# Kernel tuning notes

Measured on AMD Instinct MI355X. Metric: run time of the kernel, lower is better.

The kernel has to match this reference:

```python
import jax, jax.numpy as jnp
import numpy as np

B, S, D = 1, 2048, 1024
NH, NKV, WS = 8, 2, 64
HD = D // NH  # 128
E, HDIM, TOPK = 16, 512, 2
FP16_MIN = -65504.0
EPS = 1e-6
AUX_COEFF = 1e-5


def rmsnorm(x, w):
    return x * jax.lax.rsqrt(jnp.mean(x * x, axis=-1, keepdims=True) + EPS) * w


def setup_inputs() -> dict:
    key = jax.random.key(0)
    ks = jax.random.split(key, 24)
    r = lambda k, shape, fan: jax.random.normal(k, shape, dtype=jnp.float32) * (1.0 / np.sqrt(fan))
    return {
        "x": jax.random.normal(ks[0], (B, S, D), dtype=jnp.float32),
        "norm1_w": jnp.ones((D,), jnp.float32),
        "wq": r(ks[1], (D, NH * HD), D), "bq": jnp.zeros((NH * HD,), jnp.float32),
        "wk": r(ks[2], (D, NKV * HD), D), "bk": jnp.zeros((NKV * HD,), jnp.float32),
        "wv": r(ks[3], (D, NKV * HD), D), "bv": jnp.zeros((NKV * HD,), jnp.float32),
        "wo": r(ks[4], (NH * HD, D), NH * HD), "bo": jnp.zeros((D,), jnp.float32),
        "sink_bias": jnp.zeros((), jnp.float32),
        "norm2_w": jnp.ones((D,), jnp.float32),
        "router_w": r(ks[5], (D, E), D), "router_b": jnp.zeros((E,), jnp.float32),
        "w1": r(ks[6], (E, D, HDIM), D), "b1": jnp.zeros((E, HDIM), jnp.float32),
        "w2": r(ks[7], (E, HDIM, D), HDIM), "b2": jnp.zeros((E, D), jnp.float32),
    }


def reference(x, norm1_w, wq, bq, wk, bk, wv, bv, wo, bo, sink_bias,
              norm2_w, router_w, router_b, w1, b1, w2, b2):
    # ---- sliding-window attention with sink softmax ----
    h = rmsnorm(x, norm1_w)
    q = (h @ wq + bq).reshape(B, S, NH, HD).transpose(0, 2, 1, 3)    # [B,NH,S,HD]
    k = (h @ wk + bk).reshape(B, S, NKV, HD).transpose(0, 2, 1, 3)   # [B,NKV,S,HD]
    v = (h @ wv + bv).reshape(B, S, NKV, HD).transpose(0, 2, 1, 3)
    k = jnp.repeat(k, NH // NKV, axis=1)  # GQA expand -> [B,NH,S,HD]
    v = jnp.repeat(v, NH // NKV, axis=1)
    scores = jnp.einsum('bhqd,bhkd->bhqk', q, k) / np.sqrt(HD)
    i = jnp.arange(S)[:, None]
    j = jnp.arange(S)[None, :]
    band = (i - j >= 0) & (i - j <= WS - 1)  # causal sliding window
    scores = jnp.where(band, scores, FP16_MIN)
    m = jnp.maximum(jnp.max(scores, axis=-1, keepdims=True), sink_bias)
    ew = jnp.exp(scores - m)
    denom = jnp.sum(ew, axis=-1, keepdims=True) + jnp.exp(sink_bias - m)
    attn = ew / denom
    out = jnp.einsum('bhqk,bhkd->bhqd', attn, v).transpose(0, 2, 1, 3).reshape(B, S, D)
    x = x + (out @ wo + bo)

    # ---- MoE FFN ----
    h2 = rmsnorm(x, norm2_w)
    xf = h2.reshape(-1, D)                                  # [N,D]
    logits = (xf @ router_w + router_b) / 0.1               # [N,E]
    top_v, top_i = jax.lax.top_k(logits, TOPK)              # [N,k]
    top_w = jax.nn.softmax(top_v, axis=-1)
    probs = jax.nn.softmax(logits, axis=-1)
    aux_loss = jnp.sum(jnp.sum(probs, axis=0) ** 2) / E * AUX_COEFF
    # combine weights per (token, expert)
    gate = jnp.sum(jax.nn.one_hot(top_i, E, dtype=xf.dtype) * top_w[..., None], axis=1)  # [N,E]
    hmid = jax.nn.silu(jnp.einsum('nd,edh->neh', xf, w1) + b1)   # [N,E,H]
    y = jnp.einsum('neh,ehd->ned', hmid, w2) + b2                # [N,E,D]
    ffn = jnp.einsum('ne,ned->nd', gate, y)
    x = x + ffn.reshape(B, S, D)
    return x, aux_loss
```

## Files before the change

kernel.cpp:

```cpp
#include <hip/hip_runtime.h>
#include <hip/hip_bf16.h>

#define S     2048
#define D     1024
#define NH    8
#define NKV   2
#define HD    128
#define WS_   64
#define E_    16
#define HDIM  512
#define TOPK  2
#define NTOK  S
#define NSLOT (S*TOPK)
#define QKV_M (D + 2*NKV*HD)
#define KOFF  D
#define VOFF  (D + NKV*HD)
#define QB    8
#define WROWS (QB + WS_ - 1)
#define KPITCH 73
#define VPADF  132

typedef __attribute__((ext_vector_type(8))) short bf16x8;
typedef __attribute__((ext_vector_type(4))) float floatx4;

__device__ inline short f2bf(float f) {
    __hip_bfloat16 b = __float2bfloat16(f);
    return *reinterpret_cast<short*>(&b);
}

__global__ __launch_bounds__(256) void tconv_all(
    const float* __restrict__ wq, const float* __restrict__ wk,
    const float* __restrict__ wv, const float* __restrict__ wo,
    const float* __restrict__ w1, const float* __restrict__ w2,
    const float* __restrict__ bq, const float* __restrict__ bk,
    const float* __restrict__ bv, const float* __restrict__ router_w,
    short* __restrict__ wqkvT, short* __restrict__ woT,
    short* __restrict__ w1T, short* __restrict__ w2T,
    float* __restrict__ bqkv, float* __restrict__ rwT,
    const float* __restrict__ x, const float* __restrict__ norm1_w,
    short* __restrict__ h_bf)
{
    int id = blockIdx.x;
    if (id >= 18982) {
        int row = id - 18982, t = threadIdx.x;
        float4 v = ((const float4*)(x + (size_t)row * D))[t];
        float ss = v.x*v.x + v.y*v.y + v.z*v.z + v.w*v.w;
        #pragma unroll
        for (int off = 32; off; off >>= 1) ss += __shfl_xor(ss, off, 64);
        __shared__ float red[4];
        if ((t & 63) == 0) red[t >> 6] = ss;
        __syncthreads();
        float total = red[0] + red[1] + red[2] + red[3];
        float scale = rsqrtf(total * (1.0f / (float)D) + 1e-6f);
        float4 wv4 = ((const float4*)norm1_w)[t];
        short4 ob;
        ob.x = f2bf(v.x * scale * wv4.x); ob.y = f2bf(v.y * scale * wv4.y);
        ob.z = f2bf(v.z * scale * wv4.z); ob.w = f2bf(v.w * scale * wv4.w);
        ((short4*)(h_bf + (size_t)row * D))[t] = ob;
        return;
    }
    if (id >= 18950) {
        int ky = id - 18950;
        int t = threadIdx.x;
        int r = t >> 4, c = t & 15;
        int k0 = ky * 32;
        rwT[c * D + k0 + r]      = router_w[(k0 + r) * E_ + c];
        rwT[c * D + k0 + r + 16] = router_w[(k0 + r + 16) * E_ + c];
        return;
    }
    if (id >= 18944) {
        int t = (id - 18944) * 256 + threadIdx.x;
        if (t < D) bqkv[t] = bq[t];
        else if (t < VOFF) bqkv[t] = bk[t - D];
        else bqkv[t] = bv[t - VOFF];
        return;
    }
    const float* in; short* outp; int K, M, mx, ky;
    if (id < 1024)      { in = wq; outp = wqkvT;                  K = D; M = D;   int l = id;        mx = l & 31; ky = l >> 5; }
    else if (id < 1280) { in = wk; outp = wqkvT + (size_t)KOFF*D; K = D; M = 256; int l = id - 1024; mx = l & 7;  ky = l >> 3; }
    else if (id < 1536) { in = wv; outp = wqkvT + (size_t)VOFF*D; K = D; M = 256; int l = id - 1280; mx = l & 7;  ky = l >> 3; }
    else if (id < 2560) { in = wo; outp = woT;                    K = D; M = D;   int l = id - 1536; mx = l & 31; ky = l >> 5; }
    else if (id < 10752){ int l = id - 2560;  int e = l >> 9; int r = l & 511;
                          in = w1 + (size_t)e * D * HDIM; outp = w1T + (size_t)e * D * HDIM;
                          K = D; M = HDIM; mx = r & 15; ky = r >> 4; }
    else                { int l = id - 10752; int e = l >> 9; int r = l & 511;
                          in = w2 + (size_t)e * D * HDIM; outp = w2T + (size_t)e * D * HDIM;
                          K = HDIM; M = D; mx = r & 31; ky = r >> 5; }
    __shared__ float tile[32][33];
    int t = threadIdx.x, r = t >> 3, c4 = (t & 7) * 4;
    int k0 = ky * 32, m0 = mx * 32;
    float4 v = *(const float4*)&in[(size_t)(k0 + r) * M + m0 + c4];
    tile[r][c4 + 0] = v.x; tile[r][c4 + 1] = v.y;
    tile[r][c4 + 2] = v.z; tile[r][c4 + 3] = v.w;
    __syncthreads();
    short4 o;
    o.x = f2bf(tile[c4 + 0][r]);
    o.y = f2bf(tile[c4 + 1][r]);
    o.z = f2bf(tile[c4 + 2][r]);
    o.w = f2bf(tile[c4 + 3][r]);
    *(short4*)&outp[(size_t)(m0 + r) * K + k0 + c4] = o;
}

#define BT   64
#define BKS  64
#define BUFS (BT * BKS)

__device__ inline void gld16(const short* g, short* l) {
    __builtin_amdgcn_global_load_lds(
        (const __attribute__((address_space(1))) unsigned int*)g,
        (__attribute__((address_space(3))) unsigned int*)l, 16, 0, 0);
}

template <int V>
__global__ __launch_bounds__(256) void mgemm(
    const short* __restrict__ A, const short* __restrict__ Bt,
    const float* __restrict__ bias, float* __restrict__ C,
    short* __restrict__ Cb, const float* __restrict__ res, int K, int M,
    const int* __restrict__ offs, const float* __restrict__ tok_gate,
    const int* __restrict__ tok_map)
{
    int e = (V >= 2) ? blockIdx.z : 0;
    const short* Bte = (V >= 2) ? Bt + (size_t)e * M * K : Bt;
    const float* be  = (V >= 2) ? bias + (size_t)e * M : bias;

    int row_lo, row_hi;
    if (V >= 2) {
        row_lo = offs[e] + blockIdx.y * BT;
        row_hi = offs[e + 1];
        if (row_lo >= row_hi) return;
    } else {
        row_lo = blockIdx.y * BT;
        row_hi = 1 << 30;
    }
    int col0 = blockIdx.x * BT;

    __shared__ __align__(16) short As[2 * BUFS];
    __shared__ __align__(16) short Bs[2 * BUFS];

    int t = threadIdx.x;
    int wave = t >> 6, lane = t & 63;
    int lrow   = lane >> 3;
    int schunk = (lane & 7) ^ lrow;

    const short* aQ[2];
    const short* bQ[2];
    #pragma unroll
    for (int q = 0; q < 2; ++q) {
        int row = q * 32 + wave * 8 + lrow;
        int gr = row_lo + row;
        if (V >= 2 && gr >= row_hi) gr = row_lo;
        const short* arow;
        if (V == 2) arow = A + (size_t)(tok_map[gr] & (NTOK - 1)) * K;
        else        arow = A + (size_t)gr * K;
        aQ[q] = arow + (schunk << 3);
        bQ[q] = Bte + (size_t)(col0 + row) * K + (schunk << 3);
    }

    int rin = lane & 15, quad = lane >> 4;
    int wm = (wave & 1) * 32, wn = (wave >> 1) * 32;

    floatx4 acc[2][2];
    #pragma unroll
    for (int i = 0; i < 2; ++i)
        #pragma unroll
        for (int j = 0; j < 2; ++j)
            acc[i][j] = (floatx4){0.f, 0.f, 0.f, 0.f};

    const int NIT = K >> 6;

    #pragma unroll
    for (int q = 0; q < 2; ++q) {
        gld16(aQ[q], &As[(q * 32 + wave * 8) * BKS]);
        gld16(bQ[q], &Bs[(q * 32 + wave * 8) * BKS]);
    }
    __syncthreads();

    for (int it = 0; it < NIT; ++it) {
        int cur = it & 1, nxt = cur ^ 1;
        if (it + 1 < NIT) {
            int kk = (it + 1) << 6;
            #pragma unroll
            for (int q = 0; q < 2; ++q) {
                gld16(aQ[q] + kk, &As[nxt * BUFS + (q * 32 + wave * 8) * BKS]);
                gld16(bQ[q] + kk, &Bs[nxt * BUFS + (q * 32 + wave * 8) * BKS]);
            }
        }
        const short* Ab = &As[cur * BUFS];
        const short* Bb = &Bs[cur * BUFS];
        #pragma unroll
        for (int s = 0; s < 2; ++s) {
            bf16x8 af[2], bfr[2];
            #pragma unroll
            for (int i = 0; i < 2; ++i) {
                int row = wm + i * 16 + rin;
                af[i] = *(const bf16x8*)&Ab[row * BKS
                        + ((((s << 2) | quad) ^ (rin & 7)) << 3)];
            }
            #pragma unroll
            for (int j = 0; j < 2; ++j) {
                int row = wn + j * 16 + rin;
                bfr[j] = *(const bf16x8*)&Bb[row * BKS
                        + ((((s << 2) | quad) ^ (rin & 7)) << 3)];
            }
            #pragma unroll
            for (int i = 0; i < 2; ++i)
                #pragma unroll
                for (int j = 0; j < 2; ++j)
                    acc[i][j] = __builtin_amdgcn_mfma_f32_16x16x32_bf16(
                        af[i], bfr[j], acc[i][j], 0, 0, 0);
        }
        __syncthreads();
    }

    #pragma unroll
    for (int i = 0; i < 2; ++i) {
        #pragma unroll
        for (int j = 0; j < 2; ++j) {
            int cg = col0 + wn + j * 16 + rin;
            #pragma unroll
            for (int rr = 0; rr < 4; ++rr) {
                int rg = row_lo + wm + i * 16 + quad * 4 + rr;
                float val = acc[i][j][rr];
                if (V == 0) {
                    C[(size_t)rg * M + cg] = val + be[cg];
                } else if (V == 1) {
                    C[(size_t)rg * M + cg] = val + be[cg] + res[(size_t)rg * M + cg];
                } else if (V == 2) {
                    if (rg < row_hi) {
                        float vb_ = val + be[cg];
                        Cb[(size_t)rg * M + cg] = f2bf(vb_ / (1.f + __expf(-vb_)));
                    }
                } else {
                    if (rg < row_hi) {
                        int tok = tok_map[rg] & (NTOK - 1);
                        unsafeAtomicAdd(&C[(size_t)tok * M + cg],
                                        tok_gate[rg] * (val + be[cg]));
                    }
                }
            }
        }
    }
}

__global__ __launch_bounds__(256) void attn_kernel(
    const float* __restrict__ qkv, const float* __restrict__ sink_ptr,
    short* __restrict__ ao)
{
    __shared__ __align__(16) float KT[32 * KPITCH * 4];
    __shared__ __align__(16) float Vs[WROWS * VPADF];
    __shared__ __align__(16) float Ps4[4][64][4];

    int qblk = blockIdx.x;
    int kvh  = blockIdx.y;
    int q0   = qblk * QB;
    int jbase = q0 - (WS_ - 1);

    int t = threadIdx.x;
    int c4 = (t & 31) * 4, c4g = t & 31;
    for (int r = t >> 5; r < WROWS; r += 8) {
        int j = jbase + r;
        float4 kv4 = make_float4(0.f, 0.f, 0.f, 0.f);
        float4 vv4 = make_float4(0.f, 0.f, 0.f, 0.f);
        if (j >= 0) {
            kv4 = *(const float4*)(qkv + (size_t)j * QKV_M + KOFF + kvh * HD + c4);
            vv4 = *(const float4*)(qkv + (size_t)j * QKV_M + VOFF + kvh * HD + c4);
        }
        *(float4*)&KT[(c4g * KPITCH + r) * 4] = kv4;
        *(float4*)&Vs[r * VPADF + c4] = vv4;
    }
    __syncthreads();

    int lane = t & 63, wv = t >> 6;
    float sink = sink_ptr[0];
    const float rscale = 0.08838834764831845f;

    #pragma unroll
    for (int g = 0; g < 2; ++g) {
        int qi = wv * 2 + g;
        int i  = q0 + qi;
        bool valid = (jbase + qi + lane) >= 0;

        float sc[4] = {0.f, 0.f, 0.f, 0.f};
        const float* qbase = qkv + (size_t)i * QKV_M + (kvh * 4) * HD;
        #pragma unroll
        for (int c = 0; c < 32; ++c) {
            float4 kx = *(const float4*)&KT[(c * KPITCH + qi + lane) * 4];
            #pragma unroll
            for (int hh = 0; hh < 4; ++hh) {
                float4 q4 = *(const float4*)(qbase + hh * HD + c * 4);
                sc[hh] += q4.x*kx.x + q4.y*kx.y + q4.z*kx.z + q4.w*kx.w;
            }
        }

        float pn[4];
        #pragma unroll
        for (int hh = 0; hh < 4; ++hh) {
            float s = valid ? sc[hh] * rscale : -1e30f;
            float m = s;
            #pragma unroll
            for (int off = 32; off; off >>= 1) m = fmaxf(m, __shfl_xor(m, off, 64));
            float mf = fmaxf(m, sink);
            float p  = __expf(s - mf);
            float ds = p;
            #pragma unroll
            for (int off = 32; off; off >>= 1) ds += __shfl_xor(ds, off, 64);
            pn[hh] = p / (ds + __expf(sink - mf));
        }
        *(float4*)&Ps4[wv][lane][0] = make_float4(pn[0], pn[1], pn[2], pn[3]);

        float o0=0,o1=0,o2=0,o3=0,o4=0,o5=0,o6=0,o7=0;
        const float* vp = &Vs[qi * VPADF + 2 * lane];
        #pragma unroll
        for (int jj = 0; jj < 64; ++jj) {
            float4 p4 = *(const float4*)&Ps4[wv][jj][0];
            float2 vv = *(const float2*)(vp + jj * VPADF);
            o0 += p4.x * vv.x; o1 += p4.x * vv.y;
            o2 += p4.y * vv.x; o3 += p4.y * vv.y;
            o4 += p4.z * vv.x; o5 += p4.z * vv.y;
            o6 += p4.w * vv.x; o7 += p4.w * vv.y;
        }
        short2 r0; r0.x = f2bf(o0); r0.y = f2bf(o1);
        short2 r1; r1.x = f2bf(o2); r1.y = f2bf(o3);
        short2 r2; r2.x = f2bf(o4); r2.y = f2bf(o5);
        short2 r3; r3.x = f2bf(o6); r3.y = f2bf(o7);
        ((short2*)(ao + (size_t)i * D + (kvh * 4 + 0) * HD))[lane] = r0;
        ((short2*)(ao + (size_t)i * D + (kvh * 4 + 1) * HD))[lane] = r1;
        ((short2*)(ao + (size_t)i * D + (kvh * 4 + 2) * HD))[lane] = r2;
        ((short2*)(ao + (size_t)i * D + (kvh * 4 + 3) * HD))[lane] = r3;
    }
}

__global__ __launch_bounds__(256) void rms_router_kernel(
    const float* __restrict__ x1, const float* __restrict__ w,
    short* __restrict__ h2b, const float* __restrict__ rwT,
    const float* __restrict__ rb, float* __restrict__ probs,
    int* __restrict__ top_i, float* __restrict__ top_g,
    float* __restrict__ out)
{
    int tok = blockIdx.x, t = threadIdx.x;
    __shared__ float hrow[D];
    float4 v = ((const float4*)(x1 + (size_t)tok * D))[t];
    ((float4*)(out + (size_t)tok * D))[t] = v;
    float ss = v.x*v.x + v.y*v.y + v.z*v.z + v.w*v.w;
    #pragma unroll
    for (int off = 32; off; off >>= 1) ss += __shfl_xor(ss, off, 64);
    __shared__ float red[4];
    if ((t & 63) == 0) red[t >> 6] = ss;
    __syncthreads();
    float total = red[0] + red[1] + red[2] + red[3];
    float scale = rsqrtf(total * (1.0f / (float)D) + 1e-6f);
    float4 wv = ((const float4*)w)[t];
    float4 o;
    o.x = v.x * scale * wv.x; o.y = v.y * scale * wv.y;
    o.z = v.z * scale * wv.z; o.w = v.w * scale * wv.w;
    ((float4*)hrow)[t] = o;
    short4 ob;
    ob.x = f2bf(o.x); ob.y = f2bf(o.y); ob.z = f2bf(o.z); ob.w = f2bf(o.w);
    ((short4*)(h2b + (size_t)tok * D))[t] = ob;
    __syncthreads();

    int e = t & 15, seg = t >> 4;
    const float4* rwp = (const float4*)(rwT + (size_t)e * D + seg * 64);
    const float4* hp  = (const float4*)(hrow + seg * 64);
    float part = 0.f;
    #pragma unroll
    for (int i = 0; i < 16; ++i) {
        float4 a = hp[i];
        float4 b = rwp[i];
        part += a.x * b.x; part += a.y * b.y;
        part += a.z * b.z; part += a.w * b.w;
    }
    __shared__ float lpart[256];
    lpart[t] = part;
    __syncthreads();
    __shared__ float logits[E_];
    if (t < E_) {
        float sl = 0.f;
        for (int sg = 0; sg < 16; ++sg) sl += lpart[sg * 16 + t];
        logits[t] = (sl + rb[t]) * 10.0f;
    }
    __syncthreads();
    __shared__ float sm[2];
    if (t == 0) {
        float mx = logits[0];
        for (int x_ = 1; x_ < E_; ++x_) mx = fmaxf(mx, logits[x_]);
        float ps = 0.f;
        for (int x_ = 0; x_ < E_; ++x_) ps += __expf(logits[x_] - mx);
        sm[0] = mx; sm[1] = ps;
        int i0 = 0; float v0 = logits[0];
        for (int x_ = 1; x_ < E_; ++x_) if (logits[x_] > v0) { v0 = logits[x_]; i0 = x_; }
        int i1 = (i0 == 0) ? 1 : 0; float v1 = logits[i1];
        for (int x_ = 0; x_ < E_; ++x_) {
            if (x_ == i0) continue;
            if (logits[x_] > v1) { v1 = logits[x_]; i1 = x_; }
        }
        float e1 = __expf(v1 - v0);
        float g0 = 1.f / (1.f + e1);
        float g1 = e1 * g0;
        top_i[tok * 2 + 0] = i0; top_g[tok * 2 + 0] = g0;
        top_i[tok * 2 + 1] = i1; top_g[tok * 2 + 1] = g1;
    }
    __syncthreads();
    if (t < E_) probs[tok * E_ + t] = __expf(logits[t] - sm[0]) / sm[1];
}

__global__ __launch_bounds__(256) void finalize_scatter_kernel(
    const float* __restrict__ probs, const int* __restrict__ top_i,
    const float* __restrict__ top_g, int* __restrict__ offs,
    int* __restrict__ tok_idx, float* __restrict__ tok_gate,
    int* __restrict__ slot_of, float* __restrict__ aux_out)
{
    __shared__ float csum[E_];
    __shared__ int hist[E_];
    __shared__ int curs[E_];
    int t = threadIdx.x;
    if (t < E_) { csum[t] = 0.f; hist[t] = 0; }
    __syncthreads();

    int c = t & 15, g = t >> 4;
    float part = 0.f;
    for (int i = 0; i < NTOK / 16; ++i)
        part += probs[(size_t)(i * 16 + g) * E_ + c];
    atomicAdd(&csum[c], part);

    for (int i = 0; i < NSLOT / 256; ++i) {
        int eidx = top_i[i * 256 + t] & 15;
        atomicAdd(&hist[eidx], 1);
    }
    __syncthreads();

    if (t == 0) {
        int acc = 0;
        for (int e = 0; e < E_; ++e) { offs[e] = acc; curs[e] = acc; acc += hist[e]; }
        offs[E_] = acc;
        float s = 0.f;
        for (int e = 0; e < E_; ++e) s += csum[e] * csum[e];
        *aux_out = s / (float)E_ * 1e-5f;
    }
    __syncthreads();

    for (int i = 0; i < NTOK / 256; ++i) {
        int tok = i * 256 + t;
        #pragma unroll
        for (int s = 0; s < TOPK; ++s) {
            int e = top_i[tok * 2 + s] & 15;
            int pos = atomicAdd(&curs[e], 1) & (NSLOT - 1);
            tok_idx[pos]  = tok;
            tok_gate[pos] = top_g[tok * 2 + s];
            slot_of[tok * 2 + s] = pos;
        }
    }
}

extern "C" void kernel_launch(void* const* d_in, const int* in_sizes, int n_in,
                              void* d_out, int out_size, void* d_ws, size_t ws_size,
                              hipStream_t stream)
{
    const float* x        = (const float*)d_in[0];
    const float* norm1_w  = (const float*)d_in[1];
    const float* wq       = (const float*)d_in[2];
    const float* bq       = (const float*)d_in[3];
    const float* wk       = (const float*)d_in[4];
    const float* bk       = (const float*)d_in[5];
    const float* wv       = (const float*)d_in[6];
    const float* bv       = (const float*)d_in[7];
    const float* wo       = (const float*)d_in[8];
    const float* bo       = (const float*)d_in[9];
    const float* sink     = (const float*)d_in[10];
    const float* norm2_w  = (const float*)d_in[11];
    const float* router_w = (const float*)d_in[12];
    const float* router_b = (const float*)d_in[13];
    const float* w1       = (const float*)d_in[14];
    const float* b1       = (const float*)d_in[15];
    const float* w2       = (const float*)d_in[16];
    const float* b2       = (const float*)d_in[17];
    float* out = (float*)d_out;

    char* w = (char*)d_ws;
    auto alloc = [&](size_t bytes) {
        char* p = w; w += (bytes + 255) & ~255ull; return p;
    };
    short* wqkvT = (short*)alloc((size_t)QKV_M * D * 2);
    short* woT   = (short*)alloc((size_t)D * D * 2);
    short* w1T   = (short*)alloc((size_t)E_ * HDIM * D * 2);
    short* w2T   = (short*)alloc((size_t)E_ * D * HDIM * 2);
    float* bqkv  = (float*)alloc(QKV_M * 4);
    float* rwT   = (float*)alloc((size_t)E_ * D * 4);
    short* h_bf  = (short*)alloc((size_t)S * D * 2);
    float* qkv   = (float*)alloc((size_t)S * QKV_M * 4);
    float* x1    = (float*)alloc((size_t)S * D * 4);
    short* h2b   = (short*)alloc((size_t)S * D * 2);
    float* probs = (float*)alloc((size_t)NTOK * E_ * 4);
    int*   offs     = (int*)alloc(17 * 4);
    int*   top_i    = (int*)alloc((size_t)NSLOT * 4);
    float* top_g    = (float*)alloc((size_t)NSLOT * 4);
    int*   tok_idx  = (int*)alloc((size_t)NSLOT * 4);
    float* tok_gate = (float*)alloc((size_t)NSLOT * 4);
    int*   slot_of  = (int*)alloc((size_t)NSLOT * 4);
    short* ao_bf = h_bf;
    short* hmid  = (short*)qkv;

    tconv_all<<<21030, 256, 0, stream>>>(wq, wk, wv, wo, w1, w2, bq, bk, bv,
                                         router_w, wqkvT, woT, w1T, w2T,
                                         bqkv, rwT, x, norm1_w, h_bf);

    mgemm<0><<<dim3(QKV_M / BT, S / BT), 256, 0, stream>>>(
        h_bf, wqkvT, bqkv, qkv, nullptr, nullptr, D, QKV_M, nullptr, nullptr,
        nullptr);

    attn_kernel<<<dim3(S / QB, NKV), 256, 0, stream>>>(qkv, sink, ao_bf);

    mgemm<1><<<dim3(D / BT, S / BT), 256, 0, stream>>>(
        ao_bf, woT, bo, x1, nullptr, x, D, D, nullptr, nullptr, nullptr);

    rms_router_kernel<<<NTOK, 256, 0, stream>>>(x1, norm2_w, h2b, rwT,
                                                router_b, probs, top_i, top_g,
                                                out);

    finalize_scatter_kernel<<<1, 256, 0, stream>>>(
        probs, top_i, top_g, offs, tok_idx, tok_gate, slot_of,
        out + (size_t)S * D);

    mgemm<2><<<dim3(HDIM / BT, NSLOT / BT, E_), 256, 0, stream>>>(
        h2b, w1T, b1, nullptr, hmid, nullptr, D, HDIM, offs, nullptr, tok_idx);

    mgemm<3><<<dim3(D / BT, NSLOT / BT, E_), 256, 0, stream>>>(
        hmid, w2T, b2, out, nullptr, nullptr, HDIM, D, offs, tok_gate, tok_idx);
}
```

Before: 285.0 us.

## Triple-buffer GEMM loads, preload epilogue operands, move router reductions into atomics

```diff
diff --git a/kernel.cpp b/kernel.cpp
--- a/kernel.cpp
+++ b/kernel.cpp
@@ -38,11 +38,12 @@
     short* __restrict__ w1T, short* __restrict__ w2T,
     float* __restrict__ bqkv, float* __restrict__ rwT,
     const float* __restrict__ x, const float* __restrict__ norm1_w,
-    short* __restrict__ h_bf)
+    short* __restrict__ h_bf, float* __restrict__ gcsum,
+    int* __restrict__ ghist)
 {
     int id = blockIdx.x;
-    if (id >= 18982) {
-        int row = id - 18982, t = threadIdx.x;
+    if (id >= 18983) {
+        int row = id - 18983, t = threadIdx.x;
         float4 v = ((const float4*)(x + (size_t)row * D))[t];
         float ss = v.x*v.x + v.y*v.y + v.z*v.z + v.w*v.w;
         #pragma unroll
@@ -57,6 +58,12 @@
         ob.x = f2bf(v.x * scale * wv4.x); ob.y = f2bf(v.y * scale * wv4.y);
         ob.z = f2bf(v.z * scale * wv4.z); ob.w = f2bf(v.w * scale * wv4.w);
         ((short4*)(h_bf + (size_t)row * D))[t] = ob;
+        return;
+    }
+    if (id == 18982) {
+        int t = threadIdx.x;
+        if (t < E_) gcsum[t] = 0.f;
+        else if (t < 2 * E_) ghist[t - E_] = 0;
         return;
     }
     if (id >= 18950) {
@@ -134,8 +141,8 @@
     }
     int col0 = blockIdx.x * BT;
 
-    __shared__ __align__(16) short As[2 * BUFS];
-    __shared__ __align__(16) short Bs[2 * BUFS];
+    __shared__ __align__(16) short As[3 * BUFS];
+    __shared__ __align__(16) short Bs[3 * BUFS];
 
     int t = threadIdx.x;
     int wave = t >> 6, lane = t & 63;
@@ -159,6 +166,33 @@
     int rin = lane & 15, quad = lane >> 4;
     int wm = (wave & 1) * 32, wn = (wave >> 1) * 32;
 
+    int cg0 = col0 + wn + rin;
+    int cg1 = cg0 + 16;
+    float bj[2] = { be[cg0], be[cg1] };
+    float resv[2][2][4];
+    if (V == 1) {
+        #pragma unroll
+        for (int i = 0; i < 2; ++i)
+            #pragma unroll
+            for (int j = 0; j < 2; ++j)
+                #pragma unroll
+                for (int rr = 0; rr < 4; ++rr)
+                    resv[i][j][rr] = res[(size_t)(row_lo + wm + i*16 + quad*4 + rr) * M
+                                         + (j ? cg1 : cg0)];
+    }
+    int   tmv[2][4];
+    float tgv[2][4];
+    if (V == 3) {
+        #pragma unroll
+        for (int i = 0; i < 2; ++i)
+            #pragma unroll
+            for (int rr = 0; rr < 4; ++rr) {
+                int rg = row_lo + wm + i*16 + quad*4 + rr;
+                tmv[i][rr] = tok_map[rg] & (NTOK - 1);
+                tgv[i][rr] = tok_gate[rg];
+            }
+    }
+
     floatx4 acc[2][2];
     #pragma unroll
     for (int i = 0; i < 2; ++i)
@@ -173,20 +207,31 @@
         gld16(aQ[q], &As[(q * 32 + wave * 8) * BKS]);
         gld16(bQ[q], &Bs[(q * 32 + wave * 8) * BKS]);
     }
-    __syncthreads();
-
+    if (NIT > 1) {
+        #pragma unroll
+        for (int q = 0; q < 2; ++q) {
+            gld16(aQ[q] + 64, &As[BUFS + (q * 32 + wave * 8) * BKS]);
+            gld16(bQ[q] + 64, &Bs[BUFS + (q * 32 + wave * 8) * BKS]);
+        }
+        asm volatile("s_waitcnt vmcnt(4)\n\ts_barrier" ::: "memory");
+    } else {
+        asm volatile("s_waitcnt vmcnt(0)\n\ts_barrier" ::: "memory");
+    }
+    __builtin_amdgcn_sched_barrier(0);
+
+    int bread = 0;
     for (int it = 0; it < NIT; ++it) {
-        int cur = it & 1, nxt = cur ^ 1;
-        if (it + 1 < NIT) {
-            int kk = (it + 1) << 6;
+        if (it + 2 < NIT) {
+            int bst = bread + 2; if (bst >= 3) bst -= 3;
+            int kk = (it + 2) << 6;
             #pragma unroll
             for (int q = 0; q < 2; ++q) {
-                gld16(aQ[q] + kk, &As[nxt * BUFS + (q * 32 + wave * 8) * BKS]);
-                gld16(bQ[q] + kk, &Bs[nxt * BUFS + (q * 32 + wave * 8) * BKS]);
+                gld16(aQ[q] + kk, &As[bst * BUFS + (q * 32 + wave * 8) * BKS]);
+                gld16(bQ[q] + kk, &Bs[bst * BUFS + (q * 32 + wave * 8) * BKS]);
             }
         }
-        const short* Ab = &As[cur * BUFS];
-        const short* Bb = &Bs[cur * BUFS];
+        const short* Ab = &As[bread * BUFS];
+        const short* Bb = &Bs[bread * BUFS];
         #pragma unroll
         for (int s = 0; s < 2; ++s) {
             bf16x8 af[2], bfr[2];
@@ -209,33 +254,38 @@
                     acc[i][j] = __builtin_amdgcn_mfma_f32_16x16x32_bf16(
                         af[i], bfr[j], acc[i][j], 0, 0, 0);
         }
-        __syncthreads();
+        if (it + 1 < NIT) {
+            if (it + 2 < NIT)
+                asm volatile("s_waitcnt vmcnt(4)\n\ts_barrier" ::: "memory");
+            else
+                asm volatile("s_waitcnt vmcnt(0)\n\ts_barrier" ::: "memory");
+            __builtin_amdgcn_sched_barrier(0);
+        }
+        bread = bread + 1; if (bread >= 3) bread = 0;
     }
 
     #pragma unroll
     for (int i = 0; i < 2; ++i) {
         #pragma unroll
         for (int j = 0; j < 2; ++j) {
-            int cg = col0 + wn + j * 16 + rin;
+            int cg = j ? cg1 : cg0;
             #pragma unroll
             for (int rr = 0; rr < 4; ++rr) {
                 int rg = row_lo + wm + i * 16 + quad * 4 + rr;
                 float val = acc[i][j][rr];
                 if (V == 0) {
-                    C[(size_t)rg * M + cg] = val + be[cg];
+                    C[(size_t)rg * M + cg] = val + bj[j];
                 } else if (V == 1) {
-                    C[(size_t)rg * M + cg] = val + be[cg] + res[(size_t)rg * M + cg];
+                    C[(size_t)rg * M + cg] = val + bj[j] + resv[i][j][rr];
                 } else if (V == 2) {
                     if (rg < row_hi) {
-                        float vb_ = val + be[cg];
+                        float vb_ = val + bj[j];
                         Cb[(size_t)rg * M + cg] = f2bf(vb_ / (1.f + __expf(-vb_)));
                     }
                 } else {
-                    if (rg < row_hi) {
-                        int tok = tok_map[rg] & (NTOK - 1);
-                        unsafeAtomicAdd(&C[(size_t)tok * M + cg],
-                                        tok_gate[rg] * (val + be[cg]));
-                    }
+                    if (rg < row_hi)
+                        unsafeAtomicAdd(&C[(size_t)tmv[i][rr] * M + cg],
+                                        tgv[i][rr] * (val + bj[j]));
                 }
             }
         }
@@ -333,9 +383,9 @@
 __global__ __launch_bounds__(256) void rms_router_kernel(
     const float* __restrict__ x1, const float* __restrict__ w,
     short* __restrict__ h2b, const float* __restrict__ rwT,
-    const float* __restrict__ rb, float* __restrict__ probs,
-    int* __restrict__ top_i, float* __restrict__ top_g,
-    float* __restrict__ out)
+    const float* __restrict__ rb, float* __restrict__ gcsum,
+    int* __restrict__ ghist, int* __restrict__ top_i,
+    float* __restrict__ top_g, float* __restrict__ out)
 {
     int tok = blockIdx.x, t = threadIdx.x;
     __shared__ float hrow[D];
@@ -399,42 +449,29 @@
         float g1 = e1 * g0;
         top_i[tok * 2 + 0] = i0; top_g[tok * 2 + 0] = g0;
         top_i[tok * 2 + 1] = i1; top_g[tok * 2 + 1] = g1;
-    }
-    __syncthreads();
-    if (t < E_) probs[tok * E_ + t] = __expf(logits[t] - sm[0]) / sm[1];
+        atomicAdd(&ghist[i0], 1);
+        atomicAdd(&ghist[i1], 1);
+    }
+    __syncthreads();
+    if (t < E_)
+        unsafeAtomicAdd(&gcsum[t], __expf(logits[t] - sm[0]) / sm[1]);
 }
 
 __global__ __launch_bounds__(256) void finalize_scatter_kernel(
-    const float* __restrict__ probs, const int* __restrict__ top_i,
-    const float* __restrict__ top_g, int* __restrict__ offs,
-    int* __restrict__ tok_idx, float* __restrict__ tok_gate,
-    int* __restrict__ slot_of, float* __restrict__ aux_out)
+    const float* __restrict__ gcsum, const int* __restrict__ ghist,
+    const int* __restrict__ top_i, const float* __restrict__ top_g,
+    int* __restrict__ offs, int* __restrict__ tok_idx,
+    float* __restrict__ tok_gate, int* __restrict__ slot_of,
+    float* __restrict__ aux_out)
 {
-    __shared__ float csum[E_];
-    __shared__ int hist[E_];
     __shared__ int curs[E_];
     int t = threadIdx.x;
-    if (t < E_) { csum[t] = 0.f; hist[t] = 0; }
-    __syncthreads();
-
-    int c = t & 15, g = t >> 4;
-    float part = 0.f;
-    for (int i = 0; i < NTOK / 16; ++i)
-        part += probs[(size_t)(i * 16 + g) * E_ + c];
-    atomicAdd(&csum[c], part);
-
-    for (int i = 0; i < NSLOT / 256; ++i) {
-        int eidx = top_i[i * 256 + t] & 15;
-        atomicAdd(&hist[eidx], 1);
-    }
-    __syncthreads();
-
     if (t == 0) {
         int acc = 0;
-        for (int e = 0; e < E_; ++e) { offs[e] = acc; curs[e] = acc; acc += hist[e]; }
+        for (int e = 0; e < E_; ++e) { offs[e] = acc; curs[e] = acc; acc += ghist[e]; }
         offs[E_] = acc;
         float s = 0.f;
-        for (int e = 0; e < E_; ++e) s += csum[e] * csum[e];
+        for (int e = 0; e < E_; ++e) { float c = gcsum[e]; s += c * c; }
         *aux_out = s / (float)E_ * 1e-5f;
     }
     __syncthreads();
@@ -490,7 +527,8 @@
     float* qkv   = (float*)alloc((size_t)S * QKV_M * 4);
     float* x1    = (float*)alloc((size_t)S * D * 4);
     short* h2b   = (short*)alloc((size_t)S * D * 2);
-    float* probs = (float*)alloc((size_t)NTOK * E_ * 4);
+    float* gcsum = (float*)alloc(E_ * 4);
+    int*   ghist = (int*)alloc(E_ * 4);
     int*   offs     = (int*)alloc(17 * 4);
     int*   top_i    = (int*)alloc((size_t)NSLOT * 4);
     float* top_g    = (float*)alloc((size_t)NSLOT * 4);
@@ -500,9 +538,10 @@
     short* ao_bf = h_bf;
     short* hmid  = (short*)qkv;
 
-    tconv_all<<<21030, 256, 0, stream>>>(wq, wk, wv, wo, w1, w2, bq, bk, bv,
+    tconv_all<<<21031, 256, 0, stream>>>(wq, wk, wv, wo, w1, w2, bq, bk, bv,
                                          router_w, wqkvT, woT, w1T, w2T,
-                                         bqkv, rwT, x, norm1_w, h_bf);
+                                         bqkv, rwT, x, norm1_w, h_bf,
+                                         gcsum, ghist);
 
     mgemm<0><<<dim3(QKV_M / BT, S / BT), 256, 0, stream>>>(
         h_bf, wqkvT, bqkv, qkv, nullptr, nullptr, D, QKV_M, nullptr, nullptr,
@@ -514,11 +553,11 @@
         ao_bf, woT, bo, x1, nullptr, x, D, D, nullptr, nullptr, nullptr);
 
     rms_router_kernel<<<NTOK, 256, 0, stream>>>(x1, norm2_w, h2b, rwT,
-                                                router_b, probs, top_i, top_g,
-                                                out);
+                                                router_b, gcsum, ghist,
+                                                top_i, top_g, out);
 
     finalize_scatter_kernel<<<1, 256, 0, stream>>>(
-        probs, top_i, top_g, offs, tok_idx, tok_gate, slot_of,
+        gcsum, ghist, top_i, top_g, offs, tok_idx, tok_gate, slot_of,
         out + (size_t)S * D);
 
     mgemm<2><<<dim3(HDIM / BT, NSLOT / BT, E_), 256, 0, stream>>>(
```

Result: slower. 306.6 us (+7.6%).
